# Optimization experiments

Measured on AMD Instinct MI355X. Metric: run time of the kernel, lower is better.

The kernel has to match this reference:

```python
import jax, jax.numpy as jnp
import numpy as np

C_DIM = 768
NH = 12
MLP_HIDDEN = 3072


def _ln(x, g, b, eps=1e-5):
    mu = x.mean(-1, keepdims=True)
    var = ((x - mu) ** 2).mean(-1, keepdims=True)
    return (x - mu) / jnp.sqrt(var + eps) * g + b


def _mha(x, Wqkv, nh, scale):
    # x: [N, L, C]; Wqkv: [C, 3C] packed as (3, nh, hd) on output dim
    N, L, C = x.shape
    hd = C // nh
    qkv = (x @ Wqkv).reshape(N, L, 3, nh, hd)
    q, k, v = qkv[:, :, 0], qkv[:, :, 1], qkv[:, :, 2]  # [N, L, nh, hd]
    a = jnp.einsum('nqhd,nkhd->nhqk', q, k) * scale
    a = jax.nn.softmax(a, axis=-1)
    o = jnp.einsum('nhqk,nkhd->nqhd', a, v).reshape(N, L, C)
    return o


def setup_inputs() -> dict:
    key = jax.random.key(0)
    ks = jax.random.split(key, 16)
    B, T, K, C = 4, 16, 196, C_DIM
    s = 0.02
    inp = {
        'x': jax.random.normal(ks[0], (B, 1 + K * T, C), jnp.float32),
        'B': B, 'T': T, 'K': K,
        'ln1_g': jnp.ones((C,)), 'ln1_b': jnp.zeros((C,)),
        'lnt_g': jnp.ones((C,)), 'lnt_b': jnp.zeros((C,)),
        'ln2_g': jnp.ones((C,)), 'ln2_b': jnp.zeros((C,)),
        'lncls_g': jnp.ones((C,)), 'lncls_b': jnp.zeros((C,)),
        'Wqkv_s': jax.random.normal(ks[1], (C, 3 * C)) * s,
        'Wproj_s': jax.random.normal(ks[2], (C, C)) * s,
        'bproj_s': jnp.zeros((C,)),
        'Wqkv4': jax.random.normal(ks[3], (C, 3 * C)) * s,
        'Wqkv8': jax.random.normal(ks[4], (C, 3 * C)) * s,
        'Wqkv16': jax.random.normal(ks[5], (C, 3 * C)) * s,
        'Wp4': jax.random.normal(ks[6], (C, C)) * s, 'bp4': jnp.zeros((C,)),
        'Wp8': jax.random.normal(ks[7], (C, C)) * s, 'bp8': jnp.zeros((C,)),
        'Wp16': jax.random.normal(ks[8], (C, C)) * s, 'bp16': jnp.zeros((C,)),
        'Wtfc': jax.random.normal(ks[9], (C, C)) * s, 'btfc': jnp.zeros((C,)),
        'Wfc1': jax.random.normal(ks[10], (C, MLP_HIDDEN)) * s, 'bfc1': jnp.zeros((MLP_HIDDEN,)),
        'Wfc2': jax.random.normal(ks[11], (MLP_HIDDEN, C)) * s, 'bfc2': jnp.zeros((C,)),
    }
    return inp


def reference(x, B, T, K, ln1_g, ln1_b, lnt_g, lnt_b, ln2_g, ln2_b,
              lncls_g, lncls_b, Wqkv_s, Wproj_s, bproj_s,
              Wqkv4, Wqkv8, Wqkv16, Wp4, bp4, Wp8, bp8, Wp16, bp16,
              Wtfc, btfc, Wfc1, bfc1, Wfc2, bfc2):
    C = x.shape[-1]
    nh = NH
    scale = (C // nh) ** -0.5
    t1, t2 = T // 4, T // 2

    # ---- multi-scale temporal attention (eval mode: all dropout identity) ----
    xt = x[:, 1:, :].reshape(B, K, T, C).reshape(B * K, T, C)
    xt_n = _ln(xt, lnt_g, lnt_b)
    x4 = _mha(xt_n[:, T - t1:], Wqkv4, nh, scale) @ Wp4 + bp4    # [BK, t1, C]
    x8 = _mha(xt_n[:, t2:], Wqkv8, nh, scale) @ Wp8 + bp8        # [BK, t2, C]
    x16 = _mha(xt_n, Wqkv16, nh, scale) @ Wp16 + bp16            # [BK, T, C]
    # windowed fusion of overlapping scales
    x8 = jnp.concatenate([x8[:, :t1], 0.5 * x8[:, t1:] + 0.5 * x4], axis=1)
    x16 = jnp.concatenate([x16[:, :t2], 0.5 * x16[:, t2:] + 0.5 * x8], axis=1)
    res_temp = x16.reshape(B, K * T, C)
    xt_full = res_temp @ Wtfc + btfc + x[:, 1:, :]               # [B, K*T, C]

    # ---- spatial attention with replicated CLS token ----
    init_cls = x[:, 0:1, :]                                      # [B, 1, C]
    cls_rep = jnp.broadcast_to(init_cls, (B, T, C)).reshape(B * T, 1, C)
    xs = xt_full.reshape(B, K, T, C).transpose(0, 2, 1, 3).reshape(B * T, K, C)
    xs = jnp.concatenate([cls_rep, xs], axis=1)                  # [B*T, K+1, C]
    res_spatial = _mha(_ln(xs, ln1_g, ln1_b), Wqkv_s, nh, scale) @ Wproj_s + bproj_s

    # ---- CLS aggregation over time ----
    cls_sp = _ln(res_spatial[:, 0, :].reshape(B, T, C), lncls_g, lncls_b)
    target = cls_sp[:, -1:, :]                                   # [B, 1, C]
    attn2 = jax.nn.softmax(jnp.einsum('bqc,btc->bqt', target, cls_sp), axis=-1)
    cls_sp = attn2 @ cls_sp                                      # [B, 1, C]

    x_s = res_spatial[:, 1:, :].reshape(B, T, K, C).transpose(0, 2, 1, 3).reshape(B, K * T, C)
    x_cat = jnp.concatenate([init_cls, xt_full], axis=1) + jnp.concatenate([cls_sp, x_s], axis=1)

    # ---- MLP residual ----
    h = _ln(x_cat, ln2_g, ln2_b)
    h = jax.nn.gelu(h @ Wfc1 + bfc1, approximate=False) @ Wfc2 + bfc2
    return x_cat + h
```

## Files before the change

### kernel.cpp

```cpp
#include <hip/hip_runtime.h>
#include <hip/hip_bf16.h>
#include <stdint.h>

#define BF16 __hip_bfloat16

typedef __attribute__((ext_vector_type(8))) short short8;
typedef __attribute__((ext_vector_type(2))) short short2v;
typedef __attribute__((ext_vector_type(4))) float floatx4;

typedef const __attribute__((address_space(1))) void* gas_cvp;
typedef __attribute__((address_space(3))) void* las_vp;

__device__ __forceinline__ float bf2f(BF16 v) { return __bfloat162float(v); }
__device__ __forceinline__ BF16 f2bf(float v) { return __float2bfloat16(v); }

__global__ __launch_bounds__(256) void wtrans(const float* __restrict__ W,
                                              BF16* __restrict__ Wt, int K, int N) {
    __shared__ float t[32][33];
    int k0 = blockIdx.x * 32, n0 = blockIdx.y * 32;
    int tx = threadIdx.x & 31, ty = threadIdx.x >> 5;
#pragma unroll
    for (int i = 0; i < 32; i += 8) t[ty + i][tx] = W[(size_t)(k0 + ty + i) * N + n0 + tx];
    __syncthreads();
#pragma unroll
    for (int i = 0; i < 32; i += 8)
        Wt[(size_t)(n0 + ty + i) * K + k0 + tx] = f2bf(t[tx][ty + i]);
}

template <int MODE>
__global__ __launch_bounds__(256) void ln_kernel(const float* __restrict__ src0,
                                                 const float* __restrict__ src1,
                                                 const BF16* __restrict__ srcb,
                                                 const float* __restrict__ g,
                                                 const float* __restrict__ bta,
                                                 BF16* __restrict__ dst_bf,
                                                 float* __restrict__ dst_f) {
    const int r = blockIdx.x, tid = threadIdx.x;
    float x0, x1, x2;
    if (MODE == 3) {
        const BF16* src = srcb + (size_t)r * 197 * 768;
        x0 = bf2f(src[tid]); x1 = bf2f(src[tid + 256]); x2 = bf2f(src[tid + 512]);
    } else {
        const float* src;
        if (MODE == 0) {
            int b = r / 3136, rr = r - b * 3136;
            src = src0 + ((size_t)b * 3137 + 1 + rr) * 768;
        } else if (MODE == 1) {
            int bt = r / 197, j = r - bt * 197;
            int b = bt >> 4, t = bt & 15;
            if (j == 0) src = src0 + (size_t)b * 3137 * 768;
            else        src = src1 + ((size_t)(b * 3137 + 1) + (size_t)(j - 1) * 16 + t) * 768;
        } else {
            src = src0 + (size_t)r * 768;
        }
        x0 = src[tid]; x1 = src[tid + 256]; x2 = src[tid + 512];
    }
    float s = x0 + x1 + x2;
    float ss = x0 * x0 + x1 * x1 + x2 * x2;
    __shared__ float red[8];
#pragma unroll
    for (int o = 32; o > 0; o >>= 1) { s += __shfl_down(s, o); ss += __shfl_down(ss, o); }
    if ((tid & 63) == 0) { red[tid >> 6] = s; red[4 + (tid >> 6)] = ss; }
    __syncthreads();
    s = red[0] + red[1] + red[2] + red[3];
    ss = red[4] + red[5] + red[6] + red[7];
    const float mu = s * (1.0f / 768.0f);
    const float var = ss * (1.0f / 768.0f) - mu * mu;
    const float rstd = rsqrtf(var + 1e-5f);
#pragma unroll
    for (int i = 0; i < 3; ++i) {
        int c = tid + i * 256;
        float xv = (i == 0) ? x0 : (i == 1) ? x1 : x2;
        float y = (xv - mu) * rstd * g[c] + bta[c];
        if (MODE == 3) dst_f[(size_t)r * 768 + c] = y;
        else           dst_bf[(size_t)r * 768 + c] = f2bf(y);
    }
}

template <int AMAP, int OMODE>
__global__ __launch_bounds__(256) void gemm_bf16(const BF16* __restrict__ A,
                                                 const BF16* __restrict__ Bt,
                                                 const float* __restrict__ bias,
                                                 const void* res,
                                                 void* Cout,
                                                 int M, int N, int K) {
    __shared__ BF16 Al[128 * 64];
    __shared__ BF16 Bl[128 * 64];
    const int tid = threadIdx.x;
    const int lane = tid & 63;
    const int w = tid >> 6;
    const int bn0 = blockIdx.x * 128;
    const int bm0 = blockIdx.y * 128;

    const BF16* gsrc[8];
    BF16* ldst[8];
    const int rin = lane >> 3;
    const int kblk = (lane & 7) ^ rin;
#pragma unroll
    for (int j = 0; j < 8; ++j) {
        int c = w * 8 + j;
        if (c < 16) {
            int gr = bm0 + c * 8 + rin;
            if (gr > M - 1) gr = M - 1;
            if (AMAP == 1) gr = (gr >> 3) * 16 + 8 + (gr & 7);
            if (AMAP == 2) gr = (gr >> 2) * 16 + 12 + (gr & 3);
            gsrc[j] = A + (size_t)gr * K + kblk * 8;
            ldst[j] = Al + c * 512;
        } else {
            int gn = bn0 + (c - 16) * 8 + rin;
            gsrc[j] = Bt + (size_t)gn * K + kblk * 8;
            ldst[j] = Bl + (c - 16) * 512;
        }
    }

    const int wm = (w & 1) * 64;
    const int wn = (w >> 1) * 64;
    const int fr = lane & 15;
    const int fq = lane >> 4;
    const int sw = fr & 7;
    const int o0 = (fq ^ sw) * 8;
    const int o1 = ((fq + 4) ^ sw) * 8;
    const BF16* pa[4];
    const BF16* pb[4];
#pragma unroll
    for (int t = 0; t < 4; ++t) {
        pa[t] = Al + (wm + t * 16 + fr) * 64;
        pb[t] = Bl + (wn + t * 16 + fr) * 64;
    }

    floatx4 acc[4][4];
#pragma unroll
    for (int i = 0; i < 4; ++i)
#pragma unroll
        for (int j = 0; j < 4; ++j) acc[i][j] = (floatx4){0.f, 0.f, 0.f, 0.f};

    for (int k0 = 0; k0 < K; k0 += 64) {
#pragma unroll
        for (int j = 0; j < 8; ++j) {
            __builtin_amdgcn_global_load_lds((gas_cvp)gsrc[j], (las_vp)ldst[j], 16, 0, 0);
            gsrc[j] += 64;
        }
        __syncthreads();
        {
            short8 af[4], bfr[4];
#pragma unroll
            for (int t = 0; t < 4; ++t) {
                af[t] = *(const short8*)(pa[t] + o0);
                bfr[t] = *(const short8*)(pb[t] + o0);
            }
#pragma unroll
            for (int mt = 0; mt < 4; ++mt)
#pragma unroll
                for (int nt = 0; nt < 4; ++nt)
                    acc[mt][nt] = __builtin_amdgcn_mfma_f32_16x16x32_bf16(af[mt], bfr[nt], acc[mt][nt], 0, 0, 0);
#pragma unroll
            for (int t = 0; t < 4; ++t) {
                af[t] = *(const short8*)(pa[t] + o1);
                bfr[t] = *(const short8*)(pb[t] + o1);
            }
#pragma unroll
            for (int mt = 0; mt < 4; ++mt)
#pragma unroll
                for (int nt = 0; nt < 4; ++nt)
                    acc[mt][nt] = __builtin_amdgcn_mfma_f32_16x16x32_bf16(af[mt], bfr[nt], acc[mt][nt], 0, 0, 0);
        }
        __syncthreads();
    }

#pragma unroll
    for (int mt = 0; mt < 4; ++mt) {
#pragma unroll
        for (int nt = 0; nt < 4; ++nt) {
            const int gcol = bn0 + wn + nt * 16 + fr;
#pragma unroll
            for (int r = 0; r < 4; ++r) {
                const int grow = bm0 + wm + mt * 16 + fq * 4 + r;
                if (grow < M) {
                    float v = acc[mt][nt][r];
                    if (OMODE != 0 && OMODE != 8) v += bias[gcol];
                    if (OMODE == 0 || OMODE == 1) {
                        ((BF16*)Cout)[(size_t)grow * N + gcol] = f2bf(v);
                    } else if (OMODE == 2) {
                        int t8 = grow & 7;
                        int rr = (grow >> 3) * 16 + 8 + t8;
                        float w8 = (t8 < 4) ? 0.5f : 0.25f;
                        BF16* R = (BF16*)Cout;
                        size_t o = (size_t)rr * 768 + gcol;
                        R[o] = f2bf(0.5f * bf2f(R[o]) + w8 * v);
                    } else if (OMODE == 3) {
                        int t4 = grow & 3;
                        int rr = (grow >> 2) * 16 + 12 + t4;
                        BF16* R = (BF16*)Cout;
                        size_t o = (size_t)rr * 768 + gcol;
                        R[o] = f2bf(bf2f(R[o]) + 0.25f * v);
                    } else if (OMODE == 4) {
                        int b = grow / 3136;
                        size_t xrow = (size_t)b * 3137 + 1 + (grow - b * 3136);
                        ((float*)Cout)[xrow * 768 + gcol] =
                            v + ((const float*)res)[xrow * 768 + gcol];
                    } else if (OMODE == 6) {
                        float u = v * (0.7978845608f + 0.0356774081f * v * v);
                        v = v / (1.0f + __expf(-2.0f * u));
                        ((BF16*)Cout)[(size_t)grow * N + gcol] = f2bf(v);
                    } else {
                        v += ((const float*)res)[(size_t)grow * N + gcol];
                        ((float*)Cout)[(size_t)grow * N + gcol] = v;
                    }
                }
            }
        }
    }
}

template <int L, int NT>
__global__ __launch_bounds__(NT) void temporal_attn(const BF16* __restrict__ qkv,
                                                    BF16* __restrict__ outp) {
    __shared__ float q[L * 64];
    __shared__ float k[L * 65];
    __shared__ float v[L * 64];
    __shared__ float S[L * L];
    const int bh = blockIdx.x;
    const int b = bh / 12, h = bh % 12;
    const int tid = threadIdx.x;
    const size_t rb = (size_t)b * L;
    for (int idx = tid; idx < L * 64; idx += NT) {
        int i = idx >> 6, d = idx & 63;
        size_t base = (rb + i) * 2304 + h * 64 + d;
        q[i * 64 + d] = bf2f(qkv[base]);
        k[i * 65 + d] = bf2f(qkv[base + 768]);
        v[i * 64 + d] = bf2f(qkv[base + 1536]);
    }
    __syncthreads();
    for (int idx = tid; idx < L * L; idx += NT) {
        int i = idx / L, j = idx % L;
        float a = 0.f;
#pragma unroll
        for (int d = 0; d < 64; ++d) a += q[i * 64 + d] * k[j * 65 + d];
        S[idx] = a * 0.125f;
    }
    __syncthreads();
    if (tid < L) {
        float mx = -1e30f;
        for (int j = 0; j < L; ++j) mx = fmaxf(mx, S[tid * L + j]);
        float sm = 0.f;
        for (int j = 0; j < L; ++j) { float e = __expf(S[tid * L + j] - mx); S[tid * L + j] = e; sm += e; }
        float inv = 1.0f / sm;
        for (int j = 0; j < L; ++j) S[tid * L + j] *= inv;
    }
    __syncthreads();
    for (int idx = tid; idx < L * 64; idx += NT) {
        int i = idx >> 6, d = idx & 63;
        float acc = 0.f;
#pragma unroll
        for (int j = 0; j < L; ++j) acc += S[i * L + j] * v[j * 64 + d];
        outp[(rb + i) * 768 + h * 64 + d] = f2bf(acc);
    }
}

__global__ __launch_bounds__(256) void spatial_attn_mfma(const BF16* __restrict__ qkv,
                                                         BF16* __restrict__ outp) {
    const int bid = blockIdx.x;
    const int qt = bid & 3;
    const int h = (bid >> 2) % 12;
    const int bt = bid / 48;
    const int rowbase = bt * 197;
    __shared__ BF16 Ks[208 * 72];
    __shared__ BF16 Vt[64 * 232];
    __shared__ BF16 Pl[4][16 * 232];
    const int tid = threadIdx.x;
    const int lane = tid & 63;
    const int w = tid >> 6;
    const int ln = lane & 15;
    const int quad = lane >> 4;

    for (int it = tid; it < 208 * 8; it += 256) {
        int key = it >> 3, c = it & 7;
        int kc = key < 197 ? key : 196;
        short8 gk = *(const short8*)(qkv + (size_t)(rowbase + kc) * 2304 + 768 + h * 64 + c * 8);
        *(short8*)&Ks[key * 72 + c * 8] = gk;
    }
    for (int it = tid; it < 112 * 8; it += 256) {
        int p = it >> 3, c = it & 7;
        int kc0 = (2 * p < 197) ? 2 * p : 196;
        int kc1 = (2 * p + 1 < 197) ? 2 * p + 1 : 196;
        short8 a = *(const short8*)(qkv + (size_t)(rowbase + kc0) * 2304 + 1536 + h * 64 + c * 8);
        short8 b = *(const short8*)(qkv + (size_t)(rowbase + kc1) * 2304 + 1536 + h * 64 + c * 8);
#pragma unroll
        for (int e = 0; e < 8; ++e) {
            short2v pr;
            pr[0] = a[e];
            pr[1] = b[e];
            *(short2v*)&Vt[(c * 8 + e) * 232 + 2 * p] = pr;
        }
    }
    __syncthreads();

    const int m0 = qt * 64 + w * 16;
    int qrow = m0 + ln; if (qrow > 196) qrow = 196;
    const BF16* qptr = qkv + (size_t)(rowbase + qrow) * 2304 + h * 64 + quad * 8;
    short8 aq0 = *(const short8*)(qptr);
    short8 aq1 = *(const short8*)(qptr + 32);

    floatx4 sacc[13];
#pragma unroll
    for (int nt = 0; nt < 13; ++nt) sacc[nt] = (floatx4){0.f, 0.f, 0.f, 0.f};
#pragma unroll
    for (int nt = 0; nt < 13; ++nt) {
        const BF16* kb = &Ks[(nt * 16 + ln) * 72 + quad * 8];
        short8 b0 = *(const short8*)kb;
        short8 b1 = *(const short8*)(kb + 32);
        sacc[nt] = __builtin_amdgcn_mfma_f32_16x16x32_bf16(aq0, b0, sacc[nt], 0, 0, 0);
        sacc[nt] = __builtin_amdgcn_mfma_f32_16x16x32_bf16(aq1, b1, sacc[nt], 0, 0, 0);
    }

#pragma unroll
    for (int r = 0; r < 4; ++r) {
        float mx = -1e30f;
#pragma unroll
        for (int nt = 0; nt < 13; ++nt) {
            float s = sacc[nt][r] * 0.125f;
            sacc[nt][r] = s;
            if (nt * 16 + ln < 197) mx = fmaxf(mx, s);
        }
        mx = fmaxf(mx, __shfl_xor(mx, 1));
        mx = fmaxf(mx, __shfl_xor(mx, 2));
        mx = fmaxf(mx, __shfl_xor(mx, 4));
        mx = fmaxf(mx, __shfl_xor(mx, 8));
        float sum = 0.f;
#pragma unroll
        for (int nt = 0; nt < 13; ++nt) {
            float e = (nt * 16 + ln < 197) ? __expf(sacc[nt][r] - mx) : 0.f;
            sacc[nt][r] = e;
            sum += e;
        }
        sum += __shfl_xor(sum, 1);
        sum += __shfl_xor(sum, 2);
        sum += __shfl_xor(sum, 4);
        sum += __shfl_xor(sum, 8);
        float inv = 1.0f / sum;
#pragma unroll
        for (int nt = 0; nt < 13; ++nt) sacc[nt][r] *= inv;
    }

    BF16* pw = Pl[w];
#pragma unroll
    for (int nt = 0; nt < 13; ++nt)
#pragma unroll
        for (int r = 0; r < 4; ++r)
            pw[(quad * 4 + r) * 232 + nt * 16 + ln] = f2bf(sacc[nt][r]);
#pragma unroll
    for (int r = 0; r < 4; ++r)
        pw[(quad * 4 + r) * 232 + 208 + ln] = f2bf(0.f);

    floatx4 oacc[4];
#pragma unroll
    for (int nt = 0; nt < 4; ++nt) oacc[nt] = (floatx4){0.f, 0.f, 0.f, 0.f};
    for (int kb = 0; kb < 7; ++kb) {
        short8 ap = *(const short8*)&pw[ln * 232 + kb * 32 + quad * 8];
#pragma unroll
        for (int nt = 0; nt < 4; ++nt) {
            short8 bv = *(const short8*)&Vt[(nt * 16 + ln) * 232 + kb * 32 + quad * 8];
            oacc[nt] = __builtin_amdgcn_mfma_f32_16x16x32_bf16(ap, bv, oacc[nt], 0, 0, 0);
        }
    }

#pragma unroll
    for (int nt = 0; nt < 4; ++nt) {
        int dim = nt * 16 + ln;
#pragma unroll
        for (int r = 0; r < 4; ++r) {
            int q = m0 + quad * 4 + r;
            if (q < 197)
                outp[(size_t)(rowbase + q) * 768 + h * 64 + dim] = f2bf(oacc[nt][r]);
        }
    }
}

__global__ __launch_bounds__(256) void cls_attn_kernel(const float* __restrict__ clsln,
                                                       float* __restrict__ clsout) {
    const int b = blockIdx.x;
    const int tid = threadIdx.x;
    __shared__ float dots[16];
    __shared__ float aw[16];
    const int t = tid >> 4, l16 = tid & 15;
    const float* tgt = clsln + (size_t)(b * 16 + 15) * 768;
    const float* row = clsln + (size_t)(b * 16 + t) * 768;
    float p = 0.f;
    for (int c = l16; c < 768; c += 16) p += tgt[c] * row[c];
#pragma unroll
    for (int o = 8; o > 0; o >>= 1) p += __shfl_down(p, o, 16);
    if (l16 == 0) dots[t] = p;
    __syncthreads();
    if (tid == 0) {
        float mx = -1e30f;
        for (int j = 0; j < 16; ++j) mx = fmaxf(mx, dots[j]);
        float s = 0.f;
        for (int j = 0; j < 16; ++j) { aw[j] = __expf(dots[j] - mx); s += aw[j]; }
        float inv = 1.0f / s;
        for (int j = 0; j < 16; ++j) aw[j] *= inv;
    }
    __syncthreads();
    for (int c = tid; c < 768; c += 256) {
        float acc = 0.f;
#pragma unroll
        for (int j = 0; j < 16; ++j) acc += aw[j] * clsln[(size_t)(b * 16 + j) * 768 + c];
        clsout[(size_t)b * 768 + c] = acc;
    }
}

__global__ __launch_bounds__(256) void xcat_kernel(const float* __restrict__ x,
                                                   const BF16* __restrict__ res_sp,
                                                   const float* __restrict__ clsout,
                                                   float* outbuf) {
    const int gidx = blockIdx.x;
    const int b = gidx / 3137, j = gidx - b * 3137;
    const int tid = threadIdx.x;
    if (j == 0) {
        const float* xr = x + (size_t)b * 3137 * 768;
        const float* cr = clsout + (size_t)b * 768;
#pragma unroll
        for (int i = 0; i < 3; ++i) {
            int c = tid + i * 256;
            outbuf[(size_t)gidx * 768 + c] = xr[c] + cr[c];
        }
    } else {
        const int p = j - 1, k = p >> 4, t = p & 15;
        const BF16* rs = res_sp + (size_t)((b * 16 + t) * 197 + 1 + k) * 768;
#pragma unroll
        for (int i = 0; i < 3; ++i) {
            int c = tid + i * 256;
            outbuf[(size_t)gidx * 768 + c] = outbuf[(size_t)gidx * 768 + c] + bf2f(rs[c]);
        }
    }
}

extern "C" void kernel_launch(void* const* d_in, const int* in_sizes, int n_in,
                              void* d_out, int out_size, void* d_ws, size_t ws_size,
                              hipStream_t stream) {
    const float* x       = (const float*)d_in[0];
    const float* ln1_g   = (const float*)d_in[4];
    const float* ln1_b   = (const float*)d_in[5];
    const float* lnt_g   = (const float*)d_in[6];
    const float* lnt_b   = (const float*)d_in[7];
    const float* ln2_g   = (const float*)d_in[8];
    const float* ln2_b   = (const float*)d_in[9];
    const float* lncls_g = (const float*)d_in[10];
    const float* lncls_b = (const float*)d_in[11];
    const float* Wqkv_s  = (const float*)d_in[12];
    const float* Wproj_s = (const float*)d_in[13];
    const float* bproj_s = (const float*)d_in[14];
    const float* Wqkv4   = (const float*)d_in[15];
    const float* Wqkv8   = (const float*)d_in[16];
    const float* Wqkv16  = (const float*)d_in[17];
    const float* Wp4     = (const float*)d_in[18];
    const float* bp4     = (const float*)d_in[19];
    const float* Wp8     = (const float*)d_in[20];
    const float* bp8     = (const float*)d_in[21];
    const float* Wp16    = (const float*)d_in[22];
    const float* bp16    = (const float*)d_in[23];
    const float* Wtfc    = (const float*)d_in[24];
    const float* btfc    = (const float*)d_in[25];
    const float* Wfc1    = (const float*)d_in[26];
    const float* bfc1    = (const float*)d_in[27];
    const float* Wfc2    = (const float*)d_in[28];
    const float* bfc2    = (const float*)d_in[29];
    float* out = (float*)d_out;

    const size_t oW0 = 0;
    const size_t oW1 = 4718592;
    const size_t oR1 = 9437184;
    const size_t oR2 = 28803072;
    const size_t oR3 = 48070656;
    const size_t oR4 = 77119488;
    const size_t oCL = 96485376;
    const size_t oCO = 96681984;
    const size_t NEED = 96694272;
    if (ws_size < NEED) return;
    char* ws = (char*)d_ws;

    BF16* w0       = (BF16*)(ws + oW0);
    BF16* w1       = (BF16*)(ws + oW1);
    BF16* xtn      = (BF16*)(ws + oR1);
    BF16* atts     = (BF16*)(ws + oR1);
    BF16* hln      = (BF16*)(ws + oR1);
    BF16* res_temp = (BF16*)(ws + oR2);
    BF16* h1       = (BF16*)(ws + oR2);
    BF16* qkv      = (BF16*)(ws + oR3);
    BF16* att      = (BF16*)(ws + oR4);
    BF16* xsn      = (BF16*)(ws + oR4);
    BF16* res_sp   = (BF16*)(ws + oR4);
    float* clsln   = (float*)(ws + oCL);
    float* clsout  = (float*)(ws + oCO);

    ln_kernel<0><<<12544, 256, 0, stream>>>(x, nullptr, nullptr, lnt_g, lnt_b, xtn, nullptr);

    wtrans<<<dim3(24, 72), 256, 0, stream>>>(Wqkv16, w0, 768, 2304);
    for (int c = 0; c < 2; ++c) {
        gemm_bf16<0, 0><<<dim3(18, 49), 256, 0, stream>>>(xtn + (size_t)c * 6272 * 768, w0, nullptr, nullptr, qkv, 6272, 2304, 768);
        temporal_attn<16, 256><<<4704, 256, 0, stream>>>(qkv, att + (size_t)c * 6272 * 768);
    }
    wtrans<<<dim3(24, 24), 256, 0, stream>>>(Wp16, w1, 768, 768);
    gemm_bf16<0, 1><<<dim3(6, 98), 256, 0, stream>>>(att, w1, bp16, nullptr, res_temp, 12544, 768, 768);

    wtrans<<<dim3(24, 72), 256, 0, stream>>>(Wqkv8, w0, 768, 2304);
    gemm_bf16<1, 0><<<dim3(18, 49), 256, 0, stream>>>(xtn, w0, nullptr, nullptr, qkv, 6272, 2304, 768);
    temporal_attn<8, 64><<<9408, 64, 0, stream>>>(qkv, att);
    wtrans<<<dim3(24, 24), 256, 0, stream>>>(Wp8, w1, 768, 768);
    gemm_bf16<0, 2><<<dim3(6, 49), 256, 0, stream>>>(att, w1, bp8, nullptr, res_temp, 6272, 768, 768);

    wtrans<<<dim3(24, 72), 256, 0, stream>>>(Wqkv4, w0, 768, 2304);
    gemm_bf16<2, 0><<<dim3(18, 25), 256, 0, stream>>>(xtn, w0, nullptr, nullptr, qkv, 3136, 2304, 768);
    temporal_attn<4, 64><<<9408, 64, 0, stream>>>(qkv, att);
    wtrans<<<dim3(24, 24), 256, 0, stream>>>(Wp4, w1, 768, 768);
    gemm_bf16<0, 3><<<dim3(6, 25), 256, 0, stream>>>(att, w1, bp4, nullptr, res_temp, 3136, 768, 768);

    wtrans<<<dim3(24, 24), 256, 0, stream>>>(Wtfc, w0, 768, 768);
    gemm_bf16<0, 4><<<dim3(6, 98), 256, 0, stream>>>(res_temp, w0, btfc, x, out, 12544, 768, 768);

    ln_kernel<1><<<12608, 256, 0, stream>>>(x, out, nullptr, ln1_g, ln1_b, xsn, nullptr);
    wtrans<<<dim3(24, 72), 256, 0, stream>>>(Wqkv_s, w1, 768, 2304);
    for (int c = 0; c < 2; ++c) {
        gemm_bf16<0, 0><<<dim3(18, 50), 256, 0, stream>>>(xsn + (size_t)c * 6304 * 768, w1, nullptr, nullptr, qkv, 6304, 2304, 768);
        spatial_attn_mfma<<<1536, 256, 0, stream>>>(qkv, atts + (size_t)c * 6304 * 768);
    }
    wtrans<<<dim3(24, 24), 256, 0, stream>>>(Wproj_s, w0, 768, 768);
    gemm_bf16<0, 1><<<dim3(6, 99), 256, 0, stream>>>(atts, w0, bproj_s, nullptr, res_sp, 12608, 768, 768);

    ln_kernel<3><<<64, 256, 0, stream>>>(nullptr, nullptr, res_sp, lncls_g, lncls_b, nullptr, clsln);
    cls_attn_kernel<<<4, 256, 0, stream>>>(clsln, clsout);

    xcat_kernel<<<12548, 256, 0, stream>>>(x, res_sp, clsout, out);
    ln_kernel<2><<<12548, 256, 0, stream>>>(out, nullptr, nullptr, ln2_g, ln2_b, hln, nullptr);

    wtrans<<<dim3(24, 96), 256, 0, stream>>>(Wfc1, w0, 768, 3072);
    wtrans<<<dim3(48, 24), 256, 0, stream>>>(Wfc2, w1, 1536, 768);
    wtrans<<<dim3(48, 24), 256, 0, stream>>>(Wfc2 + (size_t)1536 * 768, w1 + (size_t)768 * 1536, 1536, 768);

    gemm_bf16<0, 6><<<dim3(12, 99), 256, 0, stream>>>(hln, w0, bfc1, nullptr, h1, 12548, 1536, 768);
    gemm_bf16<0, 7><<<dim3(6, 99), 256, 0, stream>>>(h1, w1, bfc2, out, out, 12548, 768, 1536);
    gemm_bf16<0, 6><<<dim3(12, 99), 256, 0, stream>>>(hln, w0 + (size_t)1536 * 768, bfc1 + 1536, nullptr, h1, 12548, 1536, 768);
    gemm_bf16<0, 8><<<dim3(6, 99), 256, 0, stream>>>(h1, w1 + (size_t)768 * 1536, nullptr, out, out, 12548, 768, 1536);
}
```

Measured before the change: 1.076 ms.

## Double-buffer GEMM LDS tiles and switch to 32x32x16 MFMA

Moves the bf16 GEMM main loop to two LDS buffers. The next K-tile is fetched by global_load_lds into the alternate buffer while MFMAs run on the current one, which removes one barrier per iteration and overlaps load latency with compute. The per-wave 64x64 tile now uses four 32x32x16 MFMAs per k-step instead of sixteen 16x16x32 ones, and the epilogue row/column mapping is rewritten to match. LDS use doubles to 64KB per block, which can lower occupancy. Correctness depends on the single barrier being enough to protect buffer reuse.

```diff
diff --git a/kernel.cpp b/kernel.cpp
--- a/kernel.cpp
+++ b/kernel.cpp
@@ -7,6 +7,7 @@
 typedef __attribute__((ext_vector_type(8))) short short8;
 typedef __attribute__((ext_vector_type(2))) short short2v;
 typedef __attribute__((ext_vector_type(4))) float floatx4;
+typedef __attribute__((ext_vector_type(16))) float floatx16;
 
 typedef const __attribute__((address_space(1))) void* gas_cvp;
 typedef __attribute__((address_space(3))) void* las_vp;
@@ -84,8 +85,8 @@
                                                  const void* res,
                                                  void* Cout,
                                                  int M, int N, int K) {
-    __shared__ BF16 Al[128 * 64];
-    __shared__ BF16 Bl[128 * 64];
+    __shared__ BF16 Al[2][128 * 64];
+    __shared__ BF16 Bl[2][128 * 64];
     const int tid = threadIdx.x;
     const int lane = tid & 63;
     const int w = tid >> 6;
@@ -105,78 +106,81 @@
             if (AMAP == 1) gr = (gr >> 3) * 16 + 8 + (gr & 7);
             if (AMAP == 2) gr = (gr >> 2) * 16 + 12 + (gr & 3);
             gsrc[j] = A + (size_t)gr * K + kblk * 8;
-            ldst[j] = Al + c * 512;
+            ldst[j] = &Al[0][0] + c * 512;
         } else {
             int gn = bn0 + (c - 16) * 8 + rin;
             gsrc[j] = Bt + (size_t)gn * K + kblk * 8;
-            ldst[j] = Bl + (c - 16) * 512;
+            ldst[j] = &Bl[0][0] + (c - 16) * 512;
         }
     }
 
     const int wm = (w & 1) * 64;
     const int wn = (w >> 1) * 64;
-    const int fr = lane & 15;
-    const int fq = lane >> 4;
-    const int sw = fr & 7;
-    const int o0 = (fq ^ sw) * 8;
-    const int o1 = ((fq + 4) ^ sw) * 8;
-    const BF16* pa[4];
-    const BF16* pb[4];
-#pragma unroll
-    for (int t = 0; t < 4; ++t) {
-        pa[t] = Al + (wm + t * 16 + fr) * 64;
-        pb[t] = Bl + (wn + t * 16 + fr) * 64;
-    }
-
-    floatx4 acc[4][4];
-#pragma unroll
-    for (int i = 0; i < 4; ++i)
-#pragma unroll
-        for (int j = 0; j < 4; ++j) acc[i][j] = (floatx4){0.f, 0.f, 0.f, 0.f};
-
-    for (int k0 = 0; k0 < K; k0 += 64) {
-#pragma unroll
-        for (int j = 0; j < 8; ++j) {
-            __builtin_amdgcn_global_load_lds((gas_cvp)gsrc[j], (las_vp)ldst[j], 16, 0, 0);
-            gsrc[j] += 64;
-        }
+    const int cl = lane & 31;
+    const int kh = lane >> 5;
+    const int sw = cl & 7;
+    const int baseA0 = (wm + cl) * 64;
+    const int baseA1 = (wm + 32 + cl) * 64;
+    const int baseB0 = (wn + cl) * 64;
+    const int baseB1 = (wn + 32 + cl) * 64;
+
+    floatx16 acc[2][2];
+#pragma unroll
+    for (int i = 0; i < 2; ++i)
+#pragma unroll
+        for (int j = 0; j < 2; ++j)
+#pragma unroll
+            for (int e = 0; e < 16; ++e) acc[i][j][e] = 0.f;
+
+    const int nIter = K >> 6;
+#pragma unroll
+    for (int j = 0; j < 8; ++j) {
+        __builtin_amdgcn_global_load_lds((gas_cvp)gsrc[j], (las_vp)ldst[j], 16, 0, 0);
+        gsrc[j] += 64;
+    }
+
+    for (int it = 0; it < nIter; ++it) {
         __syncthreads();
-        {
-            short8 af[4], bfr[4];
-#pragma unroll
-            for (int t = 0; t < 4; ++t) {
-                af[t] = *(const short8*)(pa[t] + o0);
-                bfr[t] = *(const short8*)(pb[t] + o0);
+        const int cur = (it & 1) * 8192;
+        const int nxt = ((it + 1) & 1) * 8192;
+        const BF16* Ab = &Al[0][0] + cur;
+        const BF16* Bb = &Bl[0][0] + cur;
+        short8 afr[4][2], bfr2[4][2];
+#pragma unroll
+        for (int s = 0; s < 4; ++s) {
+            const int ko = ((s * 2 + kh) ^ sw) * 8;
+            afr[s][0] = *(const short8*)(Ab + baseA0 + ko);
+            afr[s][1] = *(const short8*)(Ab + baseA1 + ko);
+            bfr2[s][0] = *(const short8*)(Bb + baseB0 + ko);
+            bfr2[s][1] = *(const short8*)(Bb + baseB1 + ko);
+        }
+        if (it + 1 < nIter) {
+#pragma unroll
+            for (int j = 0; j < 8; ++j) {
+                __builtin_amdgcn_global_load_lds((gas_cvp)gsrc[j], (las_vp)(ldst[j] + nxt), 16, 0, 0);
+                gsrc[j] += 64;
             }
-#pragma unroll
-            for (int mt = 0; mt < 4; ++mt)
-#pragma unroll
-                for (int nt = 0; nt < 4; ++nt)
-                    acc[mt][nt] = __builtin_amdgcn_mfma_f32_16x16x32_bf16(af[mt], bfr[nt], acc[mt][nt], 0, 0, 0);
-#pragma unroll
-            for (int t = 0; t < 4; ++t) {
-                af[t] = *(const short8*)(pa[t] + o1);
-                bfr[t] = *(const short8*)(pb[t] + o1);
-            }
-#pragma unroll
-            for (int mt = 0; mt < 4; ++mt)
-#pragma unroll
-                for (int nt = 0; nt < 4; ++nt)
-                    acc[mt][nt] = __builtin_amdgcn_mfma_f32_16x16x32_bf16(af[mt], bfr[nt], acc[mt][nt], 0, 0, 0);
-        }
-        __syncthreads();
-    }
-
-#pragma unroll
-    for (int mt = 0; mt < 4; ++mt) {
-#pragma unroll
-        for (int nt = 0; nt < 4; ++nt) {
-            const int gcol = bn0 + wn + nt * 16 + fr;
-#pragma unroll
-            for (int r = 0; r < 4; ++r) {
-                const int grow = bm0 + wm + mt * 16 + fq * 4 + r;
+        }
+#pragma unroll
+        for (int s = 0; s < 4; ++s)
+#pragma unroll
+            for (int mt = 0; mt < 2; ++mt)
+#pragma unroll
+                for (int nt = 0; nt < 2; ++nt)
+                    acc[mt][nt] = __builtin_amdgcn_mfma_f32_32x32x16_bf16(afr[s][mt], bfr2[s][nt], acc[mt][nt], 0, 0, 0);
+    }
+
+    const int rh = kh * 4;
+#pragma unroll
+    for (int mt = 0; mt < 2; ++mt) {
+#pragma unroll
+        for (int nt = 0; nt < 2; ++nt) {
+            const int gcol = bn0 + wn + nt * 32 + cl;
+#pragma unroll
+            for (int reg = 0; reg < 16; ++reg) {
+                const int grow = bm0 + wm + mt * 32 + (reg & 3) + 8 * (reg >> 2) + rh;
                 if (grow < M) {
-                    float v = acc[mt][nt][r];
+                    float v = acc[mt][nt][reg];
                     if (OMODE != 0 && OMODE != 8) v += bias[gcol];
                     if (OMODE == 0 || OMODE == 1) {
                         ((BF16*)Cout)[(size_t)grow * N + gcol] = f2bf(v);
```

After: 1.166 ms. 1.08x slower.
